# Kernel tuning notes

Hardware: AMD Instinct MI355X
Metric: run time of the kernel (lower is better)

Reference implementation:

```python
import jax, jax.numpy as jnp
import numpy as np

N_NODES = 50000
N_EDGES = 1_600_000
D = 64


def setup_inputs() -> dict:
    key = jax.random.key(0)
    k1, k2, k3, k4 = jax.random.split(key, 4)
    x = jax.random.normal(k1, (N_NODES, D), dtype=jnp.float32)
    # Glorot-ish scale for the dense transform
    weight = jax.random.normal(k2, (D, D), dtype=jnp.float32) * (1.0 / np.sqrt(D))
    bias = jnp.zeros((D,), dtype=jnp.float32)
    src = jax.random.randint(k3, (N_EDGES,), 0, N_NODES, dtype=jnp.int32)
    dst = jax.random.randint(k4, (N_EDGES,), 0, N_NODES, dtype=jnp.int32)
    t = jnp.zeros((1,), dtype=jnp.float32)
    return {"t": t, "x": x, "weight": weight, "bias": bias, "src": src, "dst": dst}


def reference(t, x, weight, bias, src, dst):
    # GCDEFunc.forward(t, x) -> GCNLayer(x); dropout=0 (eval / ODE solve).
    n = x.shape[0]
    # symmetric GCN normalization: 1/sqrt(in_degree), 0 for isolated nodes
    deg = jax.ops.segment_sum(jnp.ones_like(dst, dtype=x.dtype), dst, num_segments=n)
    norm = jnp.where(deg > 0, jax.lax.rsqrt(jnp.maximum(deg, 1.0)), 0.0)[:, None]  # [N,1]
    h = x @ weight                 # [N,D] dense transform
    h = h * norm                   # src-side normalization
    # SpMM: sum messages copy_src(h) over incoming edges
    h = jax.ops.segment_sum(h[src], dst, num_segments=n)  # [N,D]
    h = h * norm + bias            # dst-side normalization + bias
    return jax.nn.softplus(h)      # smooth activation for ODE dynamics
```

## Files before the change

kernel.cpp:

```cpp
#include <hip/hip_runtime.h>
#include <hip/hip_fp16.h>

constexpr int N = 50000;
constexpr int D = 64;
constexpr int E = 1600000;
constexpr int NBUCK = (N + 255) / 256;
constexpr int CAP = 10240;
constexpr int CPT = 16;
constexpr int BUCK_BLOCKS = (E + 256 * CPT - 1) / (256 * CPT);

__global__ void k_init(int* __restrict__ cursor) {
    int t = threadIdx.x;
    if (t < NBUCK) cursor[t] = t * CAP;
}

__global__ void k_bucket(const int* __restrict__ src, const int* __restrict__ dst,
                         int* __restrict__ cursor, unsigned* __restrict__ packed) {
    __shared__ int lh[NBUCK];
    __shared__ int lb[NBUCK];
    int tid = threadIdx.x;
    for (int i = tid; i < NBUCK; i += 256) lh[i] = 0;
    __syncthreads();
    int base_e = blockIdx.x * (256 * CPT);
    unsigned pk[CPT];
    int bn[CPT], rk[CPT];
#pragma unroll
    for (int i = 0; i < CPT; ++i) {
        int e = base_e + i * 256 + tid;
        if (e < E) {
            int d = dst[e];
            int s = src[e];
            bn[i] = d >> 8;
            pk[i] = ((unsigned)d << 16) | (unsigned)s;
            rk[i] = atomicAdd(&lh[bn[i]], 1);
        } else bn[i] = -1;
    }
    __syncthreads();
    for (int i = tid; i < NBUCK; i += 256) {
        int c = lh[i];
        lb[i] = c ? atomicAdd(&cursor[i], c) : 0;
    }
    __syncthreads();
#pragma unroll
    for (int i = 0; i < CPT; ++i)
        if (bn[i] >= 0) packed[lb[bn[i]] + rk[i]] = pk[i];
}

__global__ void k_csr(const int* __restrict__ cursor, const unsigned* __restrict__ packed,
                      unsigned short* __restrict__ csr, int* __restrict__ rowptr,
                      int* __restrict__ rowend, float* __restrict__ norm) {
    __shared__ int cnt[256];
    __shared__ int sm[256];
    __shared__ int cur[256];
    int b = blockIdx.x, tid = threadIdx.x;
    if (tid < 256) cnt[tid] = 0;
    __syncthreads();
    int beg = b * CAP;
    int end = cursor[b];
    for (int j = beg + tid; j < end; j += 1024)
        atomicAdd(&cnt[(packed[j] >> 16) & 0xFF], 1);
    __syncthreads();
    if (tid < 256) sm[tid] = cnt[tid];
    __syncthreads();
    for (int off = 1; off < 256; off <<= 1) {
        int v = 0;
        if (tid < 256 && tid >= off) v = sm[tid - off];
        __syncthreads();
        if (tid < 256) sm[tid] += v;
        __syncthreads();
    }
    if (tid < 256) {
        int excl = (tid == 0) ? 0 : sm[tid - 1];
        int node = b * 256 + tid;
        if (node < N) {
            rowptr[node] = beg + excl;
            rowend[node] = beg + sm[tid];
            norm[node] = cnt[tid] ? rsqrtf((float)cnt[tid]) : 0.0f;
        }
        cur[tid] = beg + excl;
    }
    __syncthreads();
    for (int j = beg + tid; j < end; j += 1024) {
        unsigned p = packed[j];
        int slot = atomicAdd(&cur[(p >> 16) & 0xFF], 1);
        csr[slot] = (unsigned short)(p & 0xFFFFu);
    }
}

__global__ void k_gemm(const float* __restrict__ x, const float* __restrict__ W,
                       const float* __restrict__ norm, __half* __restrict__ h2) {
    __shared__ float Wl[64 * 64];
    __shared__ float xs[16][64];
    int tid = threadIdx.x;
    const float4* W4 = (const float4*)W;
    float4* Wl4 = (float4*)Wl;
    Wl4[tid] = W4[tid];
    int r = tid >> 6, d = tid & 63;
    int row = blockIdx.x * 16 + r;
    xs[r][d] = x[row * 64 + d];
    __syncthreads();
    float a = 0.0f;
#pragma unroll
    for (int k = 0; k < 64; ++k) a = fmaf(xs[r][k], Wl[k * 64 + d], a);
    h2[row * 64 + d] = __float2half(a * norm[row]);
}

__global__ void k_aggregate(const int* __restrict__ rowptr, const int* __restrict__ rowend,
                            const unsigned short* __restrict__ csr,
                            const __half* __restrict__ h2, const float* __restrict__ norm,
                            const float* __restrict__ bias, float* __restrict__ out) {
    int node = blockIdx.x * 4 + (threadIdx.x >> 6);
    int lane = threadIdx.x & 63;
    int half = lane >> 5;
    int fl = lane & 31;
    const __half2* h2v = (const __half2*)h2;
    int beg = rowptr[node];
    int end = rowend[node];
    float ax = 0.0f, ay = 0.0f, bx = 0.0f, by = 0.0f;
    int j = beg;
    for (; j + 7 < end; j += 8) {
        int s0 = csr[j + half];
        int s1 = csr[j + 2 + half];
        int s2 = csr[j + 4 + half];
        int s3 = csr[j + 6 + half];
        float2 v0 = __half22float2(h2v[s0 * 32 + fl]);
        float2 v1 = __half22float2(h2v[s1 * 32 + fl]);
        float2 v2 = __half22float2(h2v[s2 * 32 + fl]);
        float2 v3 = __half22float2(h2v[s3 * 32 + fl]);
        ax += v0.x + v2.x;  ay += v0.y + v2.y;
        bx += v1.x + v3.x;  by += v1.y + v3.y;
    }
    for (; j + 1 < end; j += 2) {
        int s = csr[j + half];
        float2 v = __half22float2(h2v[s * 32 + fl]);
        ax += v.x;  ay += v.y;
    }
    if (j < end && half == 0) {
        int s = csr[j];
        float2 v = __half22float2(h2v[s * 32 + fl]);
        ax += v.x;  ay += v.y;
    }
    ax += bx;  ay += by;
    ax += __shfl_xor(ax, 32, 64);
    ay += __shfl_xor(ay, 32, 64);
    if (half == 0) {
        float nrm = norm[node];
        float2 bs = ((const float2*)bias)[fl];
        float vx = ax * nrm + bs.x;
        float vy = ay * nrm + bs.y;
        float2 o;
        o.x = fmaxf(vx, 0.0f) + log1pf(expf(-fabsf(vx)));
        o.y = fmaxf(vy, 0.0f) + log1pf(expf(-fabsf(vy)));
        ((float2*)out)[node * 32 + fl] = o;
    }
}

extern "C" void kernel_launch(void* const* d_in, const int* in_sizes, int n_in,
                              void* d_out, int out_size, void* d_ws, size_t ws_size,
                              hipStream_t stream) {
    const float* x    = (const float*)d_in[1];
    const float* W    = (const float*)d_in[2];
    const float* bias = (const float*)d_in[3];
    const int* src = (const int*)d_in[4];
    const int* dst = (const int*)d_in[5];
    float* out = (float*)d_out;

    char* ws = (char*)d_ws;
    __half*         h2     = (__half*)(ws);
    unsigned*       packed = (unsigned*)(ws + 6400000);
    unsigned short* csr    = (unsigned short*)(ws + 14427136);
    int*            rowptr = (int*)(ws + 18440704);
    int*            rowend = (int*)(ws + 18640704);
    float*          norm   = (float*)(ws + 18840704);
    int*            cursor = (int*)(ws + 19040704);

    k_init     <<<1, 256, 0, stream>>>(cursor);
    k_bucket   <<<BUCK_BLOCKS, 256, 0, stream>>>(src, dst, cursor, packed);
    k_csr      <<<NBUCK, 1024, 0, stream>>>(cursor, packed, csr, rowptr, rowend, norm);
    k_gemm     <<<(N + 15) / 16, 1024, 0, stream>>>(x, W, norm, h2);
    k_aggregate<<<(N + 3) / 4, 256, 0, stream>>>(rowptr, rowend, csr, h2, norm, bias, out);
}
```

Before: 175.4 us.

## Stage bucket scatter and CSR fill in shared memory for coalesced writes

The bucketing kernel now does a block-local prefix scan over bucket counts and sorts its edges into shared memory by bucket, then writes each bucket's run contiguously to global memory instead of scattering individual words. The CSR build likewise fills a shared-memory staging row and copies it out with coalesced 32-bit stores. Buckets shrink from 256 to 128 nodes with a smaller capacity, and block sizes change to 512 threads. This adds a scan and extra synchronisation per block, and the smaller bucket capacity narrows the margin against overflow.

```diff
diff --git a/kernel.cpp b/kernel.cpp
--- a/kernel.cpp
+++ b/kernel.cpp
@@ -4,10 +4,12 @@
 constexpr int N = 50000;
 constexpr int D = 64;
 constexpr int E = 1600000;
-constexpr int NBUCK = (N + 255) / 256;
-constexpr int CAP = 10240;
-constexpr int CPT = 16;
-constexpr int BUCK_BLOCKS = (E + 256 * CPT - 1) / (256 * CPT);
+constexpr int NBUCK = (N + 127) / 128;
+constexpr int CAP = 4608;
+constexpr int BTHREADS = 512;
+constexpr int CPT = 8;
+constexpr int EPB = BTHREADS * CPT;
+constexpr int BUCK_BLOCKS = (E + EPB - 1) / EPB;
 
 __global__ void k_init(int* __restrict__ cursor) {
     int t = threadIdx.x;
@@ -17,74 +19,103 @@
 __global__ void k_bucket(const int* __restrict__ src, const int* __restrict__ dst,
                          int* __restrict__ cursor, unsigned* __restrict__ packed) {
     __shared__ int lh[NBUCK];
+    __shared__ int scan[BTHREADS];
     __shared__ int lb[NBUCK];
+    __shared__ unsigned stage[EPB];
     int tid = threadIdx.x;
-    for (int i = tid; i < NBUCK; i += 256) lh[i] = 0;
-    __syncthreads();
-    int base_e = blockIdx.x * (256 * CPT);
+    for (int i = tid; i < NBUCK; i += BTHREADS) lh[i] = 0;
+    __syncthreads();
+    int base_e = blockIdx.x * EPB;
     unsigned pk[CPT];
     int bn[CPT], rk[CPT];
 #pragma unroll
     for (int i = 0; i < CPT; ++i) {
-        int e = base_e + i * 256 + tid;
+        int e = base_e + i * BTHREADS + tid;
         if (e < E) {
             int d = dst[e];
             int s = src[e];
-            bn[i] = d >> 8;
+            bn[i] = d >> 7;
             pk[i] = ((unsigned)d << 16) | (unsigned)s;
             rk[i] = atomicAdd(&lh[bn[i]], 1);
         } else bn[i] = -1;
     }
     __syncthreads();
-    for (int i = tid; i < NBUCK; i += 256) {
-        int c = lh[i];
-        lb[i] = c ? atomicAdd(&cursor[i], c) : 0;
+    scan[tid] = (tid < NBUCK) ? lh[tid] : 0;
+    __syncthreads();
+    for (int off = 1; off < BTHREADS; off <<= 1) {
+        int v = (tid >= off) ? scan[tid - off] : 0;
+        __syncthreads();
+        scan[tid] += v;
+        __syncthreads();
+    }
+    if (tid < NBUCK) {
+        int c = lh[tid];
+        lb[tid] = c ? atomicAdd(&cursor[tid], c) : 0;
     }
     __syncthreads();
 #pragma unroll
-    for (int i = 0; i < CPT; ++i)
-        if (bn[i] >= 0) packed[lb[bn[i]] + rk[i]] = pk[i];
+    for (int i = 0; i < CPT; ++i) {
+        if (bn[i] >= 0) {
+            int eb = (bn[i] == 0) ? 0 : scan[bn[i] - 1];
+            stage[eb + rk[i]] = pk[i];
+        }
+    }
+    __syncthreads();
+    int tot = scan[NBUCK - 1];
+    for (int j = tid; j < tot; j += BTHREADS) {
+        unsigned v = stage[j];
+        int bk = v >> 23;
+        int eb = (bk == 0) ? 0 : scan[bk - 1];
+        packed[lb[bk] + (j - eb)] = v;
+    }
 }
 
 __global__ void k_csr(const int* __restrict__ cursor, const unsigned* __restrict__ packed,
                       unsigned short* __restrict__ csr, int* __restrict__ rowptr,
                       int* __restrict__ rowend, float* __restrict__ norm) {
-    __shared__ int cnt[256];
-    __shared__ int sm[256];
-    __shared__ int cur[256];
+    __shared__ int cnt[128];
+    __shared__ int sm[128];
+    __shared__ int cur[128];
+    __shared__ unsigned short stage[CAP];
     int b = blockIdx.x, tid = threadIdx.x;
-    if (tid < 256) cnt[tid] = 0;
+    if (tid < 128) cnt[tid] = 0;
     __syncthreads();
     int beg = b * CAP;
-    int end = cursor[b];
-    for (int j = beg + tid; j < end; j += 1024)
-        atomicAdd(&cnt[(packed[j] >> 16) & 0xFF], 1);
-    __syncthreads();
-    if (tid < 256) sm[tid] = cnt[tid];
-    __syncthreads();
-    for (int off = 1; off < 256; off <<= 1) {
+    int m = cursor[b] - beg;
+    for (int j = tid; j < m; j += 512)
+        atomicAdd(&cnt[(packed[beg + j] >> 16) & 127], 1);
+    __syncthreads();
+    if (tid < 128) sm[tid] = cnt[tid];
+    __syncthreads();
+    for (int off = 1; off < 128; off <<= 1) {
         int v = 0;
-        if (tid < 256 && tid >= off) v = sm[tid - off];
-        __syncthreads();
-        if (tid < 256) sm[tid] += v;
-        __syncthreads();
-    }
-    if (tid < 256) {
+        if (tid < 128 && tid >= off) v = sm[tid - off];
+        __syncthreads();
+        if (tid < 128) sm[tid] += v;
+        __syncthreads();
+    }
+    if (tid < 128) {
         int excl = (tid == 0) ? 0 : sm[tid - 1];
-        int node = b * 256 + tid;
+        int node = b * 128 + tid;
         if (node < N) {
             rowptr[node] = beg + excl;
             rowend[node] = beg + sm[tid];
             norm[node] = cnt[tid] ? rsqrtf((float)cnt[tid]) : 0.0f;
         }
-        cur[tid] = beg + excl;
-    }
-    __syncthreads();
-    for (int j = beg + tid; j < end; j += 1024) {
-        unsigned p = packed[j];
-        int slot = atomicAdd(&cur[(p >> 16) & 0xFF], 1);
-        csr[slot] = (unsigned short)(p & 0xFFFFu);
-    }
+        cur[tid] = excl;
+    }
+    __syncthreads();
+    for (int j = tid; j < m; j += 512) {
+        unsigned p = packed[beg + j];
+        int slot = atomicAdd(&cur[(p >> 16) & 127], 1);
+        stage[slot] = (unsigned short)(p & 0xFFFFu);
+    }
+    __syncthreads();
+    unsigned* du = (unsigned*)(csr + beg);
+    const unsigned* su = (const unsigned*)stage;
+    int mu = m >> 1;
+    for (int k = tid; k < mu; k += 512) du[k] = su[k];
+    if ((m & 1) && tid == 0) csr[beg + m - 1] = stage[m - 1];
 }
 
 __global__ void k_gemm(const float* __restrict__ x, const float* __restrict__ W,
@@ -168,15 +199,15 @@
     char* ws = (char*)d_ws;
     __half*         h2     = (__half*)(ws);
     unsigned*       packed = (unsigned*)(ws + 6400000);
-    unsigned short* csr    = (unsigned short*)(ws + 14427136);
-    int*            rowptr = (int*)(ws + 18440704);
-    int*            rowend = (int*)(ws + 18640704);
-    float*          norm   = (float*)(ws + 18840704);
-    int*            cursor = (int*)(ws + 19040704);
-
-    k_init     <<<1, 256, 0, stream>>>(cursor);
-    k_bucket   <<<BUCK_BLOCKS, 256, 0, stream>>>(src, dst, cursor, packed);
-    k_csr      <<<NBUCK, 1024, 0, stream>>>(cursor, packed, csr, rowptr, rowend, norm);
+    unsigned short* csr    = (unsigned short*)(ws + 13606912);
+    int*            rowptr = (int*)(ws + 17210368);
+    int*            rowend = (int*)(ws + 17410368);
+    float*          norm   = (float*)(ws + 17610368);
+    int*            cursor = (int*)(ws + 17810368);
+
+    k_init     <<<1, 512, 0, stream>>>(cursor);
+    k_bucket   <<<BUCK_BLOCKS, BTHREADS, 0, stream>>>(src, dst, cursor, packed);
+    k_csr      <<<NBUCK, 512, 0, stream>>>(cursor, packed, csr, rowptr, rowend, norm);
     k_gemm     <<<(N + 15) / 16, 1024, 0, stream>>>(x, W, norm, h2);
     k_aggregate<<<(N + 3) / 4, 256, 0, stream>>>(rowptr, rowend, csr, h2, norm, bias, out);
 }
```

After: 165.9 us. 1.06x faster.
